# Optimization experiments

Measured on AMD Instinct MI355X. Metric: run time of the kernel, lower is better.

## Reference

```python
import jax, jax.numpy as jnp
import numpy as np

B, S, D = 8, 1024, 512


def setup_inputs() -> dict:
    key = jax.random.key(0)
    k1, k2, k3, k4, k5, k6, k7 = jax.random.split(key, 7)
    inp = jax.random.normal(k1, (B, S, D), dtype=jnp.float32)
    aspect = jax.random.normal(k2, (B, S, D), dtype=jnp.float32)
    # lengths in [S//2, S], with max exactly S (the module requires max(len)==S)
    inp_len = jax.random.randint(k3, (B,), S // 2, S + 1).astype(jnp.float32)
    inp_len = inp_len.at[0].set(float(S))
    lim = float(np.sqrt(6.0 / (D + D)))  # xavier_uniform bound
    w1 = jax.random.uniform(k4, (D, D), jnp.float32, -lim, lim)
    b1 = jax.random.uniform(k5, (D,), jnp.float32, -lim, lim)
    w2 = jax.random.uniform(k6, (D, D), jnp.float32, -lim, lim)
    b2 = jax.random.uniform(k7, (D,), jnp.float32, -lim, lim)
    return {"inp": inp, "inp_len": inp_len, "aspect": aspect,
            "w1": w1, "b1": b1, "w2": w2, "b2": b2}


def reference(inp, inp_len, aspect, w1, b1, w2, b2):
    # inp, aspect: [B,S,D]; inp_len: [B] float lengths with max == S
    Bv, Sv, Dv = inp.shape
    scale = jnp.sqrt(inp_len)[:, None, None]                      # [B,1,1]
    att = jnp.einsum('bsd,btd->bst', aspect, inp) / scale          # [B,S,S]
    # mask over the query (row) dimension, as in the original expand
    mask = (jnp.arange(Sv)[None, :] < inp_len.astype(jnp.int32)[:, None]).astype(inp.dtype)  # [B,S]
    exp = att * mask[:, :, None]
    att_n = exp / (jnp.sum(exp, axis=-1, keepdims=True) + 1e-4)    # linear (non-exp) normalize
    weighted = jnp.einsum('bst,btd->bsd', att_n, inp)              # [B,S,D]
    ffn_inp = weighted + (inp + aspect) * mask[:, :, None]
    # FFN: two square linears with relu, plus inner residual
    o1 = jax.nn.relu(jnp.einsum('bsd,ed->bse', ffn_inp, w1) + b1)
    o2 = jax.nn.relu(jnp.einsum('bsd,ed->bse', o1, w2) + b2)
    ffn_out = o2 + ffn_inp
    final = ffn_inp + ffn_out
    return final / jnp.linalg.norm(final, axis=2, keepdims=True)
```

## Files before the change

kernel.cpp:

```cpp
#include <hip/hip_runtime.h>

#define Bq 8
#define Sq 1024
#define Dq 512

typedef __attribute__((ext_vector_type(8))) short bf16x8;
typedef __attribute__((ext_vector_type(4))) float f32x4;

__device__ __forceinline__ unsigned short f2bf(float f) {
  unsigned int u = __float_as_uint(f);
  return (unsigned short)((u + 0x7fffu + ((u >> 16) & 1u)) >> 16);
}

__device__ __forceinline__ void load_lds16(const unsigned short* g, unsigned short* l) {
  __builtin_amdgcn_global_load_lds(
      (const __attribute__((address_space(1))) unsigned int*)g,
      (__attribute__((address_space(3))) unsigned int*)l, 16, 0, 0);
}

__global__ __launch_bounds__(256) void prep_all(
    const float* __restrict__ inp, const float* __restrict__ aspect,
    const float* __restrict__ w1, const float* __restrict__ w2,
    unsigned short* __restrict__ inpT, float* __restrict__ partial,
    unsigned short* __restrict__ asp_bf,
    unsigned short* __restrict__ w1b, unsigned short* __restrict__ w2b) {
  __shared__ unsigned short tile[32][33];
  __shared__ float csum[8][33];
  int idx = blockIdx.x;
  int tid = threadIdx.x;
  if (idx < 4096) {
    int b = idx & 7;
    int tt = (idx >> 3) & 31;
    int t0 = tt * 32, d0 = (idx >> 8) * 32;
    int tx = tid & 31, ty = tid >> 5;
    const float* src = inp + ((size_t)b * Sq + t0) * Dq + d0;
    float part = 0.f;
#pragma unroll
    for (int i = 0; i < 4; ++i) {
      float v = src[(size_t)(ty + i * 8) * Dq + tx];
      tile[ty + i * 8][tx] = f2bf(v);
      part += v;
    }
    csum[ty][tx] = part;
    __syncthreads();
    unsigned short* dst = inpT + (size_t)b * Dq * Sq;
#pragma unroll
    for (int i = 0; i < 4; ++i)
      dst[(size_t)(d0 + ty + i * 8) * Sq + t0 + tx] = tile[tx][ty + i * 8];
    if (ty == 0) {
      float s = 0.f;
#pragma unroll
      for (int i = 0; i < 8; ++i) s += csum[i][tx];
      partial[((size_t)b * 32 + tt) * Dq + d0 + tx] = s;
    }
  } else if (idx < 4608) {
    int blk = idx - 4096;
    const float* s = aspect + (size_t)blk * 8192 + tid * 4;
    unsigned short* d = asp_bf + (size_t)blk * 8192 + tid * 4;
#pragma unroll
    for (int j = 0; j < 8; ++j) {
      float4 v = *(const float4*)(s + j * 1024);
      ushort4 o; o.x = f2bf(v.x); o.y = f2bf(v.y); o.z = f2bf(v.z); o.w = f2bf(v.w);
      *(ushort4*)(d + j * 1024) = o;
    }
  } else {
    int blk = idx - 4608;
    const float* src = (blk < 256) ? w1 : w2;
    unsigned short* dst = (blk < 256) ? w1b : w2b;
    int i = ((blk & 255) * 256 + tid) * 4;
    float4 v = *(const float4*)(src + i);
    ushort4 o; o.x = f2bf(v.x); o.y = f2bf(v.y); o.z = f2bf(v.z); o.w = f2bf(v.w);
    *(ushort4*)(dst + i) = o;
  }
}

__global__ __launch_bounds__(256, 5) void gram_fac(
    const unsigned short* __restrict__ inpT, const float* __restrict__ partial,
    const float* __restrict__ aspect, const float* __restrict__ lenv,
    unsigned short* __restrict__ Gm, float* __restrict__ fac) {
  __shared__ unsigned short sA[2][32 * 64];
  __shared__ unsigned short sB[2][64 * 64];
  int idx = blockIdx.x;
  int tid = threadIdx.x;
  int lane = tid & 63, wave = tid >> 6;

  if (idx >= 1024) {
    float* cs = (float*)sA;
    int fblk = idx - 1024;
    int b = fblk >> 6;
    int s0 = (fblk & 63) * 16;
#pragma unroll
    for (int h = 0; h < 2; ++h) {
      int d = h * 256 + tid;
      float s = 0.f;
      const float* p = partial + (size_t)b * 32 * Dq + d;
#pragma unroll
      for (int t = 0; t < 32; ++t) s += p[t * Dq];
      cs[d] = s;
    }
    __syncthreads();
    int g = lane >> 4, lr = lane & 15;
    int row = s0 + wave * 4 + g;
    const float* a = aspect + ((size_t)b * Sq + row) * Dq + lr * 32;
    float sum = 0.f;
#pragma unroll
    for (int j = 0; j < 8; ++j) {
      float4 v = *(const float4*)(a + j * 4);
      const float* c = cs + lr * 32 + j * 4;
      sum += v.x * c[0] + v.y * c[1] + v.z * c[2] + v.w * c[3];
    }
#pragma unroll
    for (int off = 1; off < 16; off <<= 1) sum += __shfl_xor(sum, off, 64);
    if (lr == 0) {
      float len = lenv[b];
      float scale = sqrtf(len);
      float f = 0.f;
      if (row < (int)len) f = 1.f / (scale * (sum / scale + 1e-4f));
      fac[b * Sq + row] = f;
    }
    return;
  }

  const int K = 1024;
  int b = idx & 7;
  int tile = idx >> 3;
  int bm = tile & 15, bn = tile >> 4;
  const unsigned short* Ab = inpT + (size_t)b * Dq * Sq + (size_t)bm * 32 * K;
  const unsigned short* Bb = inpT + (size_t)b * Dq * Sq + (size_t)bn * 64 * K;
  int lr = lane & 15, lq = lane >> 4;
  int x7 = lr & 7;
  int l3 = lane >> 3, l7 = lane & 7;

  const unsigned short* gA = Ab + (size_t)(wave * 8 + l3) * K + (l7 ^ l3) * 8;
  const unsigned short* gB = Bb + (size_t)(wave * 16 + l3) * K + (l7 ^ l3) * 8;
  int dbaseA = (wave * 64 + lane) * 8;
  int dbaseB0 = (wave * 128 + lane) * 8;
  int dbaseB1 = (wave * 128 + 64 + lane) * 8;

  f32x4 acc[2] = {};

  auto issue = [&](int buf, int k0) {
    load_lds16(gA + k0, &sA[buf][dbaseA]);
    load_lds16(gB + k0, &sB[buf][dbaseB0]);
    load_lds16(gB + (size_t)8 * K + k0, &sB[buf][dbaseB1]);
  };

  int wm = (wave & 1) * 16, wn = (wave >> 1) * 32;
  issue(0, 0);
#pragma unroll
  for (int it = 0; it < 16; ++it) {
    int cur = it & 1;
    __syncthreads();
    if (it + 1 < 16) issue(cur ^ 1, (it + 1) << 6);
#pragma unroll
    for (int c = 0; c < 2; ++c) {
      int g = c * 4 + lq;
      bf16x8 a0 = *(const bf16x8*)&sA[cur][((wm + lr) * 8 + (g ^ x7)) * 8];
      bf16x8 b0 = *(const bf16x8*)&sB[cur][((wn + lr) * 8 + (g ^ x7)) * 8];
      bf16x8 b1 = *(const bf16x8*)&sB[cur][((wn + 16 + lr) * 8 + (g ^ x7)) * 8];
      acc[0] = __builtin_amdgcn_mfma_f32_16x16x32_bf16(a0, b0, acc[0], 0, 0, 0);
      acc[1] = __builtin_amdgcn_mfma_f32_16x16x32_bf16(a0, b1, acc[1], 0, 0, 0);
    }
  }

  unsigned short* Ob = Gm + (size_t)b * 512 * 512;
#pragma unroll
  for (int ni = 0; ni < 2; ++ni)
#pragma unroll
    for (int i = 0; i < 4; ++i) {
      int r = bm * 32 + wm + lq * 4 + i;
      int cc = bn * 64 + wn + ni * 16 + lr;
      Ob[(size_t)r * 512 + cc] = f2bf(acc[ni][i]);
    }
}

#define LP 520
#define MEGA_SMEM (32 * LP * 2 + 2 * 32768 + 512)

__global__ __launch_bounds__(512, 2) void mega_ffn(
    const unsigned short* __restrict__ aspb, const unsigned short* __restrict__ G,
    const unsigned short* __restrict__ w1b, const unsigned short* __restrict__ w2b,
    const float* __restrict__ b1, const float* __restrict__ b2,
    const float* __restrict__ inp, const float* __restrict__ aspect,
    const float* __restrict__ fac, const float* __restrict__ lenv,
    float* __restrict__ out) {
  extern __shared__ char smem[];
  unsigned short* ldsA = (unsigned short*)smem;
  unsigned short* wbuf = (unsigned short*)(smem + 32 * LP * 2);
  float* ssqW = (float*)(smem + 32 * LP * 2 + 2 * 32768);
  int tid = threadIdx.x;
  int lane = tid & 63, wave = tid >> 6;
  int mg = wave >> 2, ng = wave & 3;
  int lr = lane & 15, lq = lane >> 4;
  int r0 = blockIdx.x * 32;
  int b = r0 >> 10;
  int c0 = ng * 128;
  int arow = r0 + mg * 16 + lr;

  bf16x8 af[16];
  f32x4 acc[8];
  f32x4 ffnv[8];

  auto stage = [&](int buf, int kc, const unsigned short* Bsrc) {
#pragma unroll
    for (int i = 0; i < 4; ++i) {
      int n = i * 128 + wave * 16 + (lane >> 2);
      load_lds16(Bsrc + (size_t)n * 512 + kc * 32 + (lane & 3) * 8,
                 wbuf + buf * 16384 + (size_t)(i * 512 + wave * 64 + lane) * 8);
    }
  };

  auto gemmPhase = [&](const unsigned short* Bsrc) {
#pragma unroll
    for (int t = 0; t < 8; ++t) acc[t] = (f32x4){0.f, 0.f, 0.f, 0.f};
    stage(0, 0, Bsrc);
#pragma unroll
    for (int kc = 0; kc < 16; ++kc) {
      int cur = kc & 1;
      __syncthreads();
      if (kc < 15) stage(cur ^ 1, kc + 1, Bsrc);
      bf16x8 bfr[8];
#pragma unroll
      for (int t = 0; t < 8; ++t)
        bfr[t] = *(const bf16x8*)&wbuf[cur * 16384 + (size_t)((c0 + t * 16 + lr) * 4 + lq) * 8];
#pragma unroll
      for (int t = 0; t < 8; ++t)
        acc[t] = __builtin_amdgcn_mfma_f32_16x16x32_bf16(af[kc], bfr[t], acc[t], 0, 0, 0);
    }
  };

#pragma unroll
  for (int j = 0; j < 16; ++j)
    af[j] = *(const bf16x8*)(aspb + (size_t)arow * 512 + j * 32 + lq * 8);
  gemmPhase(G + (size_t)b * 512 * 512);
  int len = (int)lenv[b];
  float facv[4];
#pragma unroll
  for (int i = 0; i < 4; ++i) facv[i] = fac[r0 + mg * 16 + lq * 4 + i];
#pragma unroll
  for (int t = 0; t < 8; ++t) {
#pragma unroll
    for (int i = 0; i < 4; ++i) {
      int r = r0 + mg * 16 + lq * 4 + i;
      size_t idx = (size_t)r * 512 + c0 + t * 16 + lr;
      float add = ((r & 1023) < len) ? (inp[idx] + aspect[idx]) : 0.f;
      float v = acc[t][i] * facv[i] + add;
      ffnv[t][i] = v;
      ldsA[(mg * 16 + lq * 4 + i) * LP + c0 + t * 16 + lr] = f2bf(v);
    }
  }
  __syncthreads();

#pragma unroll
  for (int j = 0; j < 16; ++j)
    af[j] = *(const bf16x8*)&ldsA[(mg * 16 + lr) * LP + j * 32 + lq * 8];
  __syncthreads();
  gemmPhase(w1b);
  float biasv[8];
#pragma unroll
  for (int t = 0; t < 8; ++t) biasv[t] = b1[c0 + t * 16 + lr];
#pragma unroll
  for (int t = 0; t < 8; ++t)
#pragma unroll
    for (int i = 0; i < 4; ++i)
      ldsA[(mg * 16 + lq * 4 + i) * LP + c0 + t * 16 + lr] =
          f2bf(fmaxf(acc[t][i] + biasv[t], 0.f));
  __syncthreads();

#pragma unroll
  for (int j = 0; j < 16; ++j)
    af[j] = *(const bf16x8*)&ldsA[(mg * 16 + lr) * LP + j * 32 + lq * 8];
  __syncthreads();
  gemmPhase(w2b);
#pragma unroll
  for (int t = 0; t < 8; ++t) biasv[t] = b2[c0 + t * 16 + lr];
  float ssq[4] = {0.f, 0.f, 0.f, 0.f};
#pragma unroll
  for (int t = 0; t < 8; ++t)
#pragma unroll
    for (int i = 0; i < 4; ++i) {
      float v = 2.f * ffnv[t][i] + fmaxf(acc[t][i] + biasv[t], 0.f);
      ffnv[t][i] = v;
      ssq[i] += v * v;
    }
#pragma unroll
  for (int off = 1; off < 16; off <<= 1)
#pragma unroll
    for (int i = 0; i < 4; ++i) ssq[i] += __shfl_xor(ssq[i], off, 64);
  if (lr == 0)
#pragma unroll
    for (int i = 0; i < 4; ++i) ssqW[(mg * 4 + ng) * 16 + lq * 4 + i] = ssq[i];
  __syncthreads();
  float rn[4];
#pragma unroll
  for (int i = 0; i < 4; ++i) {
    float s = ssqW[(mg * 4 + 0) * 16 + lq * 4 + i] + ssqW[(mg * 4 + 1) * 16 + lq * 4 + i] +
              ssqW[(mg * 4 + 2) * 16 + lq * 4 + i] + ssqW[(mg * 4 + 3) * 16 + lq * 4 + i];
    rn[i] = 1.f / sqrtf(s);
  }
#pragma unroll
  for (int t = 0; t < 8; ++t)
#pragma unroll
    for (int i = 0; i < 4; ++i) {
      int r = r0 + mg * 16 + lq * 4 + i;
      out[(size_t)r * 512 + c0 + t * 16 + lr] = ffnv[t][i] * rn[i];
    }
}

extern "C" void kernel_launch(void* const* d_in, const int* in_sizes, int n_in,
                              void* d_out, int out_size, void* d_ws, size_t ws_size,
                              hipStream_t stream) {
  const float* inp = (const float*)d_in[0];
  const float* inp_len = (const float*)d_in[1];
  const float* aspect = (const float*)d_in[2];
  const float* w1 = (const float*)d_in[3];
  const float* b1 = (const float*)d_in[4];
  const float* w2 = (const float*)d_in[5];
  const float* b2 = (const float*)d_in[6];
  float* out = (float*)d_out;

  char* W = (char*)d_ws;
  const size_t MB = 1ull << 20;
  unsigned short* asp_bf = (unsigned short*)(W + 0);
  unsigned short* inpT   = (unsigned short*)(W + 8 * MB);
  unsigned short* Gm     = (unsigned short*)(W + 16 * MB);
  unsigned short* w1bf   = (unsigned short*)(W + 20 * MB);
  unsigned short* w2bf   = (unsigned short*)(W + 20 * MB + 512 * 1024);
  float*          partial= (float*)(W + 21 * MB);
  float*          fac    = (float*)(W + 22 * MB);

  prep_all<<<5120, 256, 0, stream>>>(inp, aspect, w1, w2,
                                     inpT, partial, asp_bf, w1bf, w2bf);

  gram_fac<<<1536, 256, 0, stream>>>(inpT, partial, aspect, inp_len, Gm, fac);

  hipFuncSetAttribute((const void*)mega_ffn,
                      hipFuncAttributeMaxDynamicSharedMemorySize, MEGA_SMEM);
  mega_ffn<<<256, 512, MEGA_SMEM, stream>>>(
      asp_bf, Gm, w1bf, w2bf, b1, b2, inp, aspect, fac, inp_len, out);
}
```

Before: 154.6 us.

## Stream B fragments directly from global in FFN kernel, drop LDS weight staging

The fused FFN kernel no longer stages weight tiles through double-buffered LDS with a barrier on every k-step. Each wave now owns a 64-column slice across all 32 rows and loads its A and B fragments straight from global memory (or from LDS for A), using register double-buffering. Block IDs are remapped so consecutive blocks fall on different batches. This removes per-k barriers and about 64KB of LDS use, at the cost of redundant global reads of the weights per wave and possibly less coalesced access.

```diff
diff --git a/kernel.cpp b/kernel.cpp
--- a/kernel.cpp
+++ b/kernel.cpp
@@ -175,7 +175,6 @@
 }
 
 #define LP 520
-#define MEGA_SMEM (32 * LP * 2 + 2 * 32768 + 512)
 
 __global__ __launch_bounds__(512, 2) void mega_ffn(
     const unsigned short* __restrict__ aspb, const unsigned short* __restrict__ G,
@@ -184,127 +183,145 @@
     const float* __restrict__ inp, const float* __restrict__ aspect,
     const float* __restrict__ fac, const float* __restrict__ lenv,
     float* __restrict__ out) {
-  extern __shared__ char smem[];
-  unsigned short* ldsA = (unsigned short*)smem;
-  unsigned short* wbuf = (unsigned short*)(smem + 32 * LP * 2);
-  float* ssqW = (float*)(smem + 32 * LP * 2 + 2 * 32768);
+  __shared__ unsigned short ldsA[32 * LP];
+  __shared__ float ssqW[256];
   int tid = threadIdx.x;
   int lane = tid & 63, wave = tid >> 6;
-  int mg = wave >> 2, ng = wave & 3;
   int lr = lane & 15, lq = lane >> 4;
-  int r0 = blockIdx.x * 32;
+  int bid = ((blockIdx.x & 7) << 5) | (blockIdx.x >> 3);
+  int r0 = bid * 32;
   int b = r0 >> 10;
-  int c0 = ng * 128;
-  int arow = r0 + mg * 16 + lr;
-
-  bf16x8 af[16];
-  f32x4 acc[8];
-  f32x4 ffnv[8];
-
-  auto stage = [&](int buf, int kc, const unsigned short* Bsrc) {
+  int c0 = wave * 64;
+
+  f32x4 acc[2][4];
+  float ffnv[2][4][4];
+
+  const unsigned short* Gb = G + (size_t)b * 512 * 512;
+
+  auto gemmLoop = [&](const unsigned short* Bp, auto loadA) {
+    auto loadB = [&](int kc, bf16x8* dst) {
+#pragma unroll
+      for (int t = 0; t < 4; ++t)
+        dst[t] = *(const bf16x8*)(Bp + (size_t)(c0 + t * 16 + lr) * 512 + kc * 32 + lq * 8);
+    };
+    bf16x8 aC[2], bC[4], aN[2], bN[4];
+#pragma unroll
+    for (int mg = 0; mg < 2; ++mg)
+#pragma unroll
+      for (int t = 0; t < 4; ++t) acc[mg][t] = (f32x4){0.f, 0.f, 0.f, 0.f};
+    loadA(0, aC);
+    loadB(0, bC);
+#pragma unroll
+    for (int kc = 0; kc < 16; ++kc) {
+      if (kc < 15) {
+        loadA(kc + 1, aN);
+        loadB(kc + 1, bN);
+      }
+#pragma unroll
+      for (int t = 0; t < 4; ++t) {
+        acc[0][t] = __builtin_amdgcn_mfma_f32_16x16x32_bf16(aC[0], bC[t], acc[0][t], 0, 0, 0);
+        acc[1][t] = __builtin_amdgcn_mfma_f32_16x16x32_bf16(aC[1], bC[t], acc[1][t], 0, 0, 0);
+      }
+#pragma unroll
+      for (int m = 0; m < 2; ++m) aC[m] = aN[m];
+#pragma unroll
+      for (int t = 0; t < 4; ++t) bC[t] = bN[t];
+    }
+  };
+
+  auto loadA_g = [&](int kc, bf16x8* dst) {
+    dst[0] = *(const bf16x8*)(aspb + (size_t)(r0 + lr) * 512 + kc * 32 + lq * 8);
+    dst[1] = *(const bf16x8*)(aspb + (size_t)(r0 + 16 + lr) * 512 + kc * 32 + lq * 8);
+  };
+  auto loadA_l = [&](int kc, bf16x8* dst) {
+    dst[0] = *(const bf16x8*)&ldsA[(size_t)lr * LP + kc * 32 + lq * 8];
+    dst[1] = *(const bf16x8*)&ldsA[(size_t)(16 + lr) * LP + kc * 32 + lq * 8];
+  };
+
+  gemmLoop(Gb, loadA_g);
+  int len = (int)lenv[b];
+  float facv[2][4];
+#pragma unroll
+  for (int mg = 0; mg < 2; ++mg)
+#pragma unroll
+    for (int i = 0; i < 4; ++i) facv[mg][i] = fac[r0 + mg * 16 + lq * 4 + i];
+#pragma unroll
+  for (int mg = 0; mg < 2; ++mg)
+#pragma unroll
+    for (int t = 0; t < 4; ++t)
+#pragma unroll
+      for (int i = 0; i < 4; ++i) {
+        int rr = mg * 16 + lq * 4 + i;
+        int r = r0 + rr;
+        size_t idx = (size_t)r * 512 + c0 + t * 16 + lr;
+        float add = ((r & 1023) < len) ? (inp[idx] + aspect[idx]) : 0.f;
+        float v = acc[mg][t][i] * facv[mg][i] + add;
+        ffnv[mg][t][i] = v;
+        ldsA[rr * LP + c0 + t * 16 + lr] = f2bf(v);
+      }
+  __syncthreads();
+
+  gemmLoop(w1b, loadA_l);
+  float biasv[4];
+#pragma unroll
+  for (int t = 0; t < 4; ++t) biasv[t] = b1[c0 + t * 16 + lr];
+  __syncthreads();
+#pragma unroll
+  for (int mg = 0; mg < 2; ++mg)
+#pragma unroll
+    for (int t = 0; t < 4; ++t)
+#pragma unroll
+      for (int i = 0; i < 4; ++i) {
+        int rr = mg * 16 + lq * 4 + i;
+        ldsA[rr * LP + c0 + t * 16 + lr] = f2bf(fmaxf(acc[mg][t][i] + biasv[t], 0.f));
+      }
+  __syncthreads();
+
+  gemmLoop(w2b, loadA_l);
+#pragma unroll
+  for (int t = 0; t < 4; ++t) biasv[t] = b2[c0 + t * 16 + lr];
+  float ssq[2][4] = {{0.f, 0.f, 0.f, 0.f}, {0.f, 0.f, 0.f, 0.f}};
+#pragma unroll
+  for (int mg = 0; mg < 2; ++mg)
+#pragma unroll
+    for (int t = 0; t < 4; ++t)
+#pragma unroll
+      for (int i = 0; i < 4; ++i) {
+        float v = 2.f * ffnv[mg][t][i] + fmaxf(acc[mg][t][i] + biasv[t], 0.f);
+        ffnv[mg][t][i] = v;
+        ssq[mg][i] += v * v;
+      }
+#pragma unroll
+  for (int off = 1; off < 16; off <<= 1)
+#pragma unroll
+    for (int mg = 0; mg < 2; ++mg)
+#pragma unroll
+      for (int i = 0; i < 4; ++i) ssq[mg][i] += __shfl_xor(ssq[mg][i], off, 64);
+  if (lr == 0)
+#pragma unroll
+    for (int mg = 0; mg < 2; ++mg)
+#pragma unroll
+      for (int i = 0; i < 4; ++i) ssqW[wave * 32 + mg * 16 + lq * 4 + i] = ssq[mg][i];
+  __syncthreads();
+  float rn[2][4];
+#pragma unroll
+  for (int mg = 0; mg < 2; ++mg)
 #pragma unroll
     for (int i = 0; i < 4; ++i) {
-      int n = i * 128 + wave * 16 + (lane >> 2);
-      load_lds16(Bsrc + (size_t)n * 512 + kc * 32 + (lane & 3) * 8,
-                 wbuf + buf * 16384 + (size_t)(i * 512 + wave * 64 + lane) * 8);
-    }
-  };
-
-  auto gemmPhase = [&](const unsigned short* Bsrc) {
-#pragma unroll
-    for (int t = 0; t < 8; ++t) acc[t] = (f32x4){0.f, 0.f, 0.f, 0.f};
-    stage(0, 0, Bsrc);
-#pragma unroll
-    for (int kc = 0; kc < 16; ++kc) {
-      int cur = kc & 1;
-      __syncthreads();
-      if (kc < 15) stage(cur ^ 1, kc + 1, Bsrc);
-      bf16x8 bfr[8];
-#pragma unroll
-      for (int t = 0; t < 8; ++t)
-        bfr[t] = *(const bf16x8*)&wbuf[cur * 16384 + (size_t)((c0 + t * 16 + lr) * 4 + lq) * 8];
-#pragma unroll
-      for (int t = 0; t < 8; ++t)
-        acc[t] = __builtin_amdgcn_mfma_f32_16x16x32_bf16(af[kc], bfr[t], acc[t], 0, 0, 0);
-    }
-  };
-
-#pragma unroll
-  for (int j = 0; j < 16; ++j)
-    af[j] = *(const bf16x8*)(aspb + (size_t)arow * 512 + j * 32 + lq * 8);
-  gemmPhase(G + (size_t)b * 512 * 512);
-  int len = (int)lenv[b];
-  float facv[4];
-#pragma unroll
-  for (int i = 0; i < 4; ++i) facv[i] = fac[r0 + mg * 16 + lq * 4 + i];
-#pragma unroll
-  for (int t = 0; t < 8; ++t) {
-#pragma unroll
-    for (int i = 0; i < 4; ++i) {
-      int r = r0 + mg * 16 + lq * 4 + i;
-      size_t idx = (size_t)r * 512 + c0 + t * 16 + lr;
-      float add = ((r & 1023) < len) ? (inp[idx] + aspect[idx]) : 0.f;
-      float v = acc[t][i] * facv[i] + add;
-      ffnv[t][i] = v;
-      ldsA[(mg * 16 + lq * 4 + i) * LP + c0 + t * 16 + lr] = f2bf(v);
-    }
-  }
-  __syncthreads();
-
-#pragma unroll
-  for (int j = 0; j < 16; ++j)
-    af[j] = *(const bf16x8*)&ldsA[(mg * 16 + lr) * LP + j * 32 + lq * 8];
-  __syncthreads();
-  gemmPhase(w1b);
-  float biasv[8];
-#pragma unroll
-  for (int t = 0; t < 8; ++t) biasv[t] = b1[c0 + t * 16 + lr];
-#pragma unroll
-  for (int t = 0; t < 8; ++t)
-#pragma unroll
-    for (int i = 0; i < 4; ++i)
-      ldsA[(mg * 16 + lq * 4 + i) * LP + c0 + t * 16 + lr] =
-          f2bf(fmaxf(acc[t][i] + biasv[t], 0.f));
-  __syncthreads();
-
-#pragma unroll
-  for (int j = 0; j < 16; ++j)
-    af[j] = *(const bf16x8*)&ldsA[(mg * 16 + lr) * LP + j * 32 + lq * 8];
-  __syncthreads();
-  gemmPhase(w2b);
-#pragma unroll
-  for (int t = 0; t < 8; ++t) biasv[t] = b2[c0 + t * 16 + lr];
-  float ssq[4] = {0.f, 0.f, 0.f, 0.f};
-#pragma unroll
-  for (int t = 0; t < 8; ++t)
-#pragma unroll
-    for (int i = 0; i < 4; ++i) {
-      float v = 2.f * ffnv[t][i] + fmaxf(acc[t][i] + biasv[t], 0.f);
-      ffnv[t][i] = v;
-      ssq[i] += v * v;
-    }
-#pragma unroll
-  for (int off = 1; off < 16; off <<= 1)
-#pragma unroll
-    for (int i = 0; i < 4; ++i) ssq[i] += __shfl_xor(ssq[i], off, 64);
-  if (lr == 0)
-#pragma unroll
-    for (int i = 0; i < 4; ++i) ssqW[(mg * 4 + ng) * 16 + lq * 4 + i] = ssq[i];
-  __syncthreads();
-  float rn[4];
-#pragma unroll
-  for (int i = 0; i < 4; ++i) {
-    float s = ssqW[(mg * 4 + 0) * 16 + lq * 4 + i] + ssqW[(mg * 4 + 1) * 16 + lq * 4 + i] +
-              ssqW[(mg * 4 + 2) * 16 + lq * 4 + i] + ssqW[(mg * 4 + 3) * 16 + lq * 4 + i];
-    rn[i] = 1.f / sqrtf(s);
-  }
-#pragma unroll
-  for (int t = 0; t < 8; ++t)
-#pragma unroll
-    for (int i = 0; i < 4; ++i) {
-      int r = r0 + mg * 16 + lq * 4 + i;
-      out[(size_t)r * 512 + c0 + t * 16 + lr] = ffnv[t][i] * rn[i];
-    }
+      float s = 0.f;
+#pragma unroll
+      for (int w = 0; w < 8; ++w) s += ssqW[w * 32 + mg * 16 + lq * 4 + i];
+      rn[mg][i] = 1.f / sqrtf(s);
+    }
+#pragma unroll
+  for (int mg = 0; mg < 2; ++mg)
+#pragma unroll
+    for (int t = 0; t < 4; ++t)
+#pragma unroll
+      for (int i = 0; i < 4; ++i) {
+        int r = r0 + mg * 16 + lq * 4 + i;
+        out[(size_t)r * 512 + c0 + t * 16 + lr] = ffnv[mg][t][i] * rn[mg][i];
+      }
 }
 
 extern "C" void kernel_launch(void* const* d_in, const int* in_sizes, int n_in,
@@ -334,8 +351,6 @@
 
   gram_fac<<<1536, 256, 0, stream>>>(inpT, partial, aspect, inp_len, Gm, fac);
 
-  hipFuncSetAttribute((const void*)mega_ffn,
-                      hipFuncAttributeMaxDynamicSharedMemorySize, MEGA_SMEM);
-  mega_ffn<<<256, 512, MEGA_SMEM, stream>>>(
+  mega_ffn<<<256, 512, 0, stream>>>(
       asp_bf, Gm, w1bf, w2bf, b1, b2, inp, aspect, fac, inp_len, out);
 }
```

Result: slower. 174.8 us (+13.0%).
